# Performance work log

Measured on AMD Instinct MI355X. Metric: run time of the kernel, lower is better.

Reference implementation:

```python
import jax, jax.numpy as jnp
import numpy as np

B, T, C = 8, 1024, 1024
EPS = 1e-5
NEG_INF = -1e38


def layernorm(x, w, b):
    mu = jnp.mean(x, axis=-1, keepdims=True)
    var = jnp.var(x, axis=-1, keepdims=True)
    return (x - mu) * jax.lax.rsqrt(var + EPS) * w + b


def wkv_scan(w, u, k, v):
    """Numerically-stable RWKV-4 WKV recurrence (forward direction).
    w: [C] (negative decay), u: [C] bonus, k, v: [B, T, C]. Returns [B, T, C]."""
    kt = jnp.swapaxes(k, 0, 1)  # [T, B, C]
    vt = jnp.swapaxes(v, 0, 1)
    bsz = k.shape[0]
    a0 = jnp.zeros((bsz, C), k.dtype)
    b0 = jnp.zeros((bsz, C), k.dtype)
    p0 = jnp.full((bsz, C), NEG_INF, k.dtype)

    def step(carry, inp):
        a, b, p = carry
        kk, vv = inp
        # output at current step (with bonus u on current token)
        q = jnp.maximum(p, u + kk)
        e1 = jnp.exp(p - q)
        e2 = jnp.exp(u + kk - q)
        out = (e1 * a + e2 * vv) / (e1 * b + e2)
        # decay state and absorb current token
        q2 = jnp.maximum(p + w, kk)
        f1 = jnp.exp(p + w - q2)
        f2 = jnp.exp(kk - q2)
        return (f1 * a + f2 * vv, f1 * b + f2, q2), out

    _, outs = jax.lax.scan(step, (a0, b0, p0), (kt, vt))
    return jnp.swapaxes(outs, 0, 1)  # [B, T, C]


def setup_inputs() -> dict:
    key = jax.random.key(0)
    ks = jax.random.split(key, 12)
    s = 0.02
    d = {}
    d["x"] = jax.random.normal(ks[0], (B, T, C), jnp.float32)
    d["ln1_w"] = jnp.ones((C,), jnp.float32)
    d["ln1_b"] = jnp.zeros((C,), jnp.float32)
    d["ln2_w"] = jnp.ones((C,), jnp.float32)
    d["ln2_b"] = jnp.zeros((C,), jnp.float32)
    d["Wr"] = jax.random.normal(ks[1], (C, C), jnp.float32) * s
    d["Wk"] = jax.random.normal(ks[2], (C, C), jnp.float32) * s
    d["Wv"] = jax.random.normal(ks[3], (C, C), jnp.float32) * s
    d["Wo"] = jax.random.normal(ks[4], (C, C), jnp.float32) * s
    d["decay"] = jax.random.normal(ks[5], (C,), jnp.float32) * 0.1
    d["u"] = jax.random.normal(ks[6], (C,), jnp.float32) * 0.1
    d["Wfk"] = jax.random.normal(ks[7], (4 * C, C), jnp.float32) * s
    d["Wfv"] = jax.random.normal(ks[8], (C, 4 * C), jnp.float32) * s
    d["Wfr"] = jax.random.normal(ks[9], (C, C), jnp.float32) * s
    return d


def reference(x, ln1_w, ln1_b, ln2_w, ln2_b, Wr, Wk, Wv, Wo, decay, u, Wfk, Wfv, Wfr):
    # --- bidirectional time-mix (WKV attention) ---
    xn = layernorm(x, ln1_w, ln1_b)
    r = jax.nn.sigmoid(xn @ Wr.T)
    k = xn @ Wk.T
    v = xn @ Wv.T
    w = -jnp.exp(decay)  # per-channel negative decay
    wkv_f = wkv_scan(w, u, k, v)
    wkv_b = jnp.flip(wkv_scan(w, u, jnp.flip(k, axis=1), jnp.flip(v, axis=1)), axis=1)
    wkv = 0.5 * (wkv_f + wkv_b)
    x = x + (r * wkv) @ Wo.T
    # --- channel-mix FFN ---
    xn2 = layernorm(x, ln2_w, ln2_b)
    kk = jnp.square(jax.nn.relu(xn2 @ Wfk.T))  # [B, T, 4C]
    x = x + jax.nn.sigmoid(xn2 @ Wfr.T) * (kk @ Wfv.T)
    return x
```

## Files before the change

kernel.cpp:

```cpp
#include <hip/hip_runtime.h>
#include <cstdint>
#include <cstddef>

typedef unsigned short u16;
typedef unsigned char u8;
typedef unsigned int u32;
typedef __bf16 bf16_t;
typedef bf16_t bf16x8 __attribute__((ext_vector_type(8)));
typedef float f32x4 __attribute__((ext_vector_type(4)));
typedef int i32x8 __attribute__((ext_vector_type(8)));

#define GCH 16
#define TCH 64

static __device__ __forceinline__ float bf2f(u16 v) {
    union { unsigned int u; float f; } cv;
    cv.u = ((unsigned int)v) << 16;
    return cv.f;
}
static __device__ __forceinline__ u16 f2bf(float f) {
    union { float f; unsigned int u; } cv;
    cv.f = f;
    unsigned int r = 0x7fffu + ((cv.u >> 16) & 1u);
    return (u16)((cv.u + r) >> 16);
}

struct WSegs { const float* src[7]; void* dst[7]; int n4[7]; int mode[7]; };

__global__ __launch_bounds__(256)
void wconv_all(WSegs s)
{
    const int seg = blockIdx.y;
    const int i = blockIdx.x * 256 + threadIdx.x;
    if (i >= s.n4[seg]) return;
    float4 f = ((const float4*)s.src[seg])[i];
    if (s.mode[seg] == 0) {
        ushort4 o;
        o.x = f2bf(f.x); o.y = f2bf(f.y); o.z = f2bf(f.z); o.w = f2bf(f.w);
        ((ushort4*)s.dst[seg])[i] = o;
    } else {
        const int p0 = __builtin_amdgcn_cvt_pk_fp8_f32(f.x * 16.f, f.y * 16.f, 0, 0);
        const int p1 = __builtin_amdgcn_cvt_pk_fp8_f32(f.z * 16.f, f.w * 16.f, 0, 0);
        ((u32*)s.dst[seg])[i] = (u32)(p0 & 0xFFFF) | ((u32)p1 << 16);
    }
}

template<int BF16IN, int OUT8>
__global__ __launch_bounds__(256)
void ln_kernel(const void* __restrict__ xin, const float* __restrict__ w,
               const float* __restrict__ b, void* __restrict__ out)
{
    const int row = blockIdx.x;
    const int tid = threadIdx.x;
    float vals[4];
    if (BF16IN) {
        const ushort4 uv = ((const ushort4*)((const u16*)xin + (size_t)row * 1024))[tid];
        vals[0] = bf2f(uv.x); vals[1] = bf2f(uv.y);
        vals[2] = bf2f(uv.z); vals[3] = bf2f(uv.w);
    } else {
        const float4 f = ((const float4*)((const float*)xin + (size_t)row * 1024))[tid];
        vals[0] = f.x; vals[1] = f.y; vals[2] = f.z; vals[3] = f.w;
    }
    float s  = vals[0] + vals[1] + vals[2] + vals[3];
    float ss = vals[0]*vals[0] + vals[1]*vals[1] + vals[2]*vals[2] + vals[3]*vals[3];
    for (int off = 32; off; off >>= 1) {
        s  += __shfl_down(s, off, 64);
        ss += __shfl_down(ss, off, 64);
    }
    __shared__ float redS[4], redQ[4];
    if ((tid & 63) == 0) { redS[tid >> 6] = s; redQ[tid >> 6] = ss; }
    __syncthreads();
    s  = redS[0] + redS[1] + redS[2] + redS[3];
    ss = redQ[0] + redQ[1] + redQ[2] + redQ[3];
    const float mu  = s * (1.f / 1024.f);
    const float var = ss * (1.f / 1024.f) - mu * mu;
    const float rs  = rsqrtf(var + 1e-5f);
    const float4 wv = ((const float4*)w)[tid];
    const float4 bv = ((const float4*)b)[tid];
    const float o0 = (vals[0] - mu) * rs * wv.x + bv.x;
    const float o1 = (vals[1] - mu) * rs * wv.y + bv.y;
    const float o2 = (vals[2] - mu) * rs * wv.z + bv.z;
    const float o3 = (vals[3] - mu) * rs * wv.w + bv.w;
    if (OUT8) {
        const int p0 = __builtin_amdgcn_cvt_pk_fp8_f32(o0, o1, 0, 0);
        const int p1 = __builtin_amdgcn_cvt_pk_fp8_f32(o2, o3, 0, 0);
        ((u32*)out)[(size_t)row * 256 + tid] = (u32)(p0 & 0xFFFF) | ((u32)p1 << 16);
    } else {
        ushort4 o;
        o.x = f2bf(o0); o.y = f2bf(o1); o.z = f2bf(o2); o.w = f2bf(o3);
        ((ushort4*)out)[(size_t)row * 256 + tid] = o;
    }
}

template<int EPI, int DBUF>
__global__ __launch_bounds__(256)
void gemm_bt(const u16* __restrict__ A, const u16* __restrict__ B,
             int M, int N, int K,
             void* __restrict__ outp,
             const void* __restrict__ aux1, const void* __restrict__ aux2)
{
    __shared__ u16 lA[(1 + DBUF) * 128 * 64];
    __shared__ u16 lB[(1 + DBUF) * 128 * 64];
    const int tid  = threadIdx.x;
    const int wave = tid >> 6;
    const int lane = tid & 63;
    const int q    = lane >> 4;
    const int l16  = lane & 15;
    const long mBase = (long)blockIdx.x * 128;
    const long nBase = (long)blockIdx.y * 128;
    const int wm = (wave >> 1) * 64;
    const int wn = (wave & 1) * 64;

    f32x4 acc[4][4];
#pragma unroll
    for (int i = 0; i < 4; ++i)
#pragma unroll
        for (int j = 0; j < 4; ++j)
#pragma unroll
            for (int r = 0; r < 4; ++r) acc[i][j][r] = 0.f;

    const int srow = tid >> 3;
    const int scol = ((tid & 7) ^ (srow & 7)) * 8;
    const int ldsW = wave * 512;
    const int swz = l16 & 7;

    if (DBUF == 0) {
        for (int kb = 0; kb < K; kb += 64) {
            __syncthreads();
#pragma unroll
            for (int c = 0; c < 4; ++c) {
                const int row = c * 32 + srow;
                const u16* ga = A + (mBase + row) * (long)K + kb + scol;
                const u16* gb = B + (nBase + row) * (long)K + kb + scol;
                __builtin_amdgcn_global_load_lds(
                    (const __attribute__((address_space(1))) void*)ga,
                    (__attribute__((address_space(3))) void*)(lA + c * 2048 + ldsW),
                    16, 0, 0);
                __builtin_amdgcn_global_load_lds(
                    (const __attribute__((address_space(1))) void*)gb,
                    (__attribute__((address_space(3))) void*)(lB + c * 2048 + ldsW),
                    16, 0, 0);
            }
            __syncthreads();
#pragma unroll
            for (int ks = 0; ks < 2; ++ks) {
                const int grp = ((ks * 4 + q) ^ swz) * 8;
                bf16x8 af[4], bfm[4];
#pragma unroll
                for (int i = 0; i < 4; ++i) {
                    af[i]  = *(const bf16x8*)(lA + (wm + i * 16 + l16) * 64 + grp);
                    bfm[i] = *(const bf16x8*)(lB + (wn + i * 16 + l16) * 64 + grp);
                }
#pragma unroll
                for (int i = 0; i < 4; ++i)
#pragma unroll
                    for (int j = 0; j < 4; ++j)
                        acc[i][j] = __builtin_amdgcn_mfma_f32_16x16x32_bf16(
                            af[i], bfm[j], acc[i][j], 0, 0, 0);
            }
        }
    } else {
#pragma unroll
        for (int c = 0; c < 4; ++c) {
            const int row = c * 32 + srow;
            const u16* ga = A + (mBase + row) * (long)K + scol;
            const u16* gb = B + (nBase + row) * (long)K + scol;
            __builtin_amdgcn_global_load_lds(
                (const __attribute__((address_space(1))) void*)ga,
                (__attribute__((address_space(3))) void*)(lA + c * 2048 + ldsW),
                16, 0, 0);
            __builtin_amdgcn_global_load_lds(
                (const __attribute__((address_space(1))) void*)gb,
                (__attribute__((address_space(3))) void*)(lB + c * 2048 + ldsW),
                16, 0, 0);
        }
        __syncthreads();
        int cur = 0;
        for (int kb = 0; kb < K; kb += 64) {
            if (kb + 64 < K) {
                const int nb = (cur ^ 1) * 8192;
#pragma unroll
                for (int c = 0; c < 4; ++c) {
                    const int row = c * 32 + srow;
                    const u16* ga = A + (mBase + row) * (long)K + kb + 64 + scol;
                    const u16* gb = B + (nBase + row) * (long)K + kb + 64 + scol;
                    __builtin_amdgcn_global_load_lds(
                        (const __attribute__((address_space(1))) void*)ga,
                        (__attribute__((address_space(3))) void*)(lA + nb + c * 2048 + ldsW),
                        16, 0, 0);
                    __builtin_amdgcn_global_load_lds(
                        (const __attribute__((address_space(1))) void*)gb,
                        (__attribute__((address_space(3))) void*)(lB + nb + c * 2048 + ldsW),
                        16, 0, 0);
                }
            }
            const u16* bA = lA + cur * 8192;
            const u16* bB = lB + cur * 8192;
#pragma unroll
            for (int ks = 0; ks < 2; ++ks) {
                const int grp = ((ks * 4 + q) ^ swz) * 8;
                bf16x8 af[4], bfm[4];
#pragma unroll
                for (int i = 0; i < 4; ++i) {
                    af[i]  = *(const bf16x8*)(bA + (wm + i * 16 + l16) * 64 + grp);
                    bfm[i] = *(const bf16x8*)(bB + (wn + i * 16 + l16) * 64 + grp);
                }
#pragma unroll
                for (int i = 0; i < 4; ++i)
#pragma unroll
                    for (int j = 0; j < 4; ++j)
                        acc[i][j] = __builtin_amdgcn_mfma_f32_16x16x32_bf16(
                            af[i], bfm[j], acc[i][j], 0, 0, 0);
            }
            __syncthreads();
            cur ^= 1;
        }
    }

    if (EPI == 5) {
        const long seg = nBase >> 10;
        u16* optr = (u16*)(seg == 0 ? outp : seg == 1 ? (void*)aux1 : (void*)aux2);
        const long cb = (nBase & 1023) + wn + l16;
#pragma unroll
        for (int i = 0; i < 4; ++i)
#pragma unroll
            for (int r = 0; r < 4; ++r) {
                const long rowOff = (mBase + wm + i * 16 + q * 4 + r) * 1024 + cb;
#pragma unroll
                for (int j = 0; j < 4; ++j)
                    optr[rowOff + j * 16] = f2bf(acc[i][j][r]);
            }
    } else {
        const long colBase = nBase + wn + l16;
#pragma unroll
        for (int i = 0; i < 4; ++i) {
#pragma unroll
            for (int r = 0; r < 4; ++r) {
                const long row = mBase + wm + i * 16 + q * 4 + r;
                const long rowOff = row * (long)N;
#pragma unroll
                for (int j = 0; j < 4; ++j) {
                    const long idx = rowOff + colBase + j * 16;
                    const float val = acc[i][j][r];
                    if (EPI == 1) {
                        ((u16*)outp)[idx] = f2bf(((const float*)aux1)[idx] + val);
                    } else {
                        const float t = bf2f(((const u16*)aux1)[idx])
                                      + bf2f(((const u16*)aux2)[idx]) * val;
                        ((float*)outp)[idx] = t;
                    }
                }
            }
        }
    }
}

__global__ __launch_bounds__(256)
void gemm_f8(const u8* __restrict__ A, const u8* __restrict__ B,
             int M, int N, int K,
             u16* __restrict__ kk, u16* __restrict__ rp)
{
    __shared__ __align__(16) u8 lA[128 * 128];
    __shared__ __align__(16) u8 lB[128 * 128];
    const int tid  = threadIdx.x;
    const int wave = tid >> 6;
    const int lane = tid & 63;
    const int q    = lane >> 4;
    const int l16  = lane & 15;
    const long mBase = (long)blockIdx.x * 128;
    const long nBase = (long)blockIdx.y * 128;
    const int wm = (wave >> 1) * 64;
    const int wn = (wave & 1) * 64;

    f32x4 acc[4][4];
#pragma unroll
    for (int i = 0; i < 4; ++i)
#pragma unroll
        for (int j = 0; j < 4; ++j)
#pragma unroll
            for (int r = 0; r < 4; ++r) acc[i][j][r] = 0.f;

    const int srow  = tid >> 3;
    const int scolB = ((tid & 7) ^ (srow & 7)) * 16;
    const int ldsW  = wave * 1024;
    const int swz   = l16 & 7;

    for (int kb = 0; kb < K; kb += 128) {
        __syncthreads();
#pragma unroll
        for (int c = 0; c < 4; ++c) {
            const int row = c * 32 + srow;
            const u8* ga = A + (mBase + row) * (long)K + kb + scolB;
            const u8* gb = B + (nBase + row) * (long)K + kb + scolB;
            __builtin_amdgcn_global_load_lds(
                (const __attribute__((address_space(1))) void*)ga,
                (__attribute__((address_space(3))) void*)(lA + c * 4096 + ldsW),
                16, 0, 0);
            __builtin_amdgcn_global_load_lds(
                (const __attribute__((address_space(1))) void*)gb,
                (__attribute__((address_space(3))) void*)(lB + c * 4096 + ldsW),
                16, 0, 0);
        }
        __syncthreads();
        const int u0 = ((2 * q) ^ swz) * 16;
        const int u1 = ((2 * q + 1) ^ swz) * 16;
        i32x8 af[4], bfm[4];
#pragma unroll
        for (int i = 0; i < 4; ++i) {
            {
                const u8* base = lA + (wm + i * 16 + l16) * 128;
                const uint4 lo = *(const uint4*)(base + u0);
                const uint4 hi = *(const uint4*)(base + u1);
                af[i][0] = lo.x; af[i][1] = lo.y; af[i][2] = lo.z; af[i][3] = lo.w;
                af[i][4] = hi.x; af[i][5] = hi.y; af[i][6] = hi.z; af[i][7] = hi.w;
            }
            {
                const u8* base = lB + (wn + i * 16 + l16) * 128;
                const uint4 lo = *(const uint4*)(base + u0);
                const uint4 hi = *(const uint4*)(base + u1);
                bfm[i][0] = lo.x; bfm[i][1] = lo.y; bfm[i][2] = lo.z; bfm[i][3] = lo.w;
                bfm[i][4] = hi.x; bfm[i][5] = hi.y; bfm[i][6] = hi.z; bfm[i][7] = hi.w;
            }
        }
#pragma unroll
        for (int i = 0; i < 4; ++i)
#pragma unroll
            for (int j = 0; j < 4; ++j)
                acc[i][j] = __builtin_amdgcn_mfma_scale_f32_16x16x128_f8f6f4(
                    af[i], bfm[j], acc[i][j], 0, 0, 0, 127, 0, 123);
    }

    u16* optr; long sN, cb;
    if (nBase < 4096) { optr = kk; sN = 4096; cb = nBase + wn + l16; }
    else              { optr = rp; sN = 1024; cb = (nBase - 4096) + wn + l16; }
#pragma unroll
    for (int i = 0; i < 4; ++i)
#pragma unroll
        for (int r = 0; r < 4; ++r) {
            const long rowOff = (mBase + wm + i * 16 + q * 4 + r) * sN + cb;
#pragma unroll
            for (int j = 0; j < 4; ++j) {
                const float val = acc[i][j][r];
                float t;
                if (nBase < 4096) t = val > 0.f ? val * val : 0.f;
                else t = __fdividef(1.f, 1.f + __expf(-val));
                optr[rowOff + j * 16] = f2bf(t);
            }
        }
}

__global__ __launch_bounds__(64)
void wkv_sum(const u16* __restrict__ kbuf, const u16* __restrict__ vbuf,
             const float* __restrict__ decay,
             float* __restrict__ sumA, float* __restrict__ sumB,
             float* __restrict__ sumP)
{
    const int c   = blockIdx.x * 64 + threadIdx.x;
    const int bt  = blockIdx.y;
    const int dir = blockIdx.z & 1;
    const int g   = blockIdx.z >> 1;
    const long base = (long)bt * (1024 * 1024) + c;
    const long stride = dir ? -1024 : 1024;
    long idx = dir ? base + (long)(1023 - g * TCH) * 1024
                   : base + (long)(g * TCH) * 1024;
    const float w = -__expf(decay[c]);
    float a = 0.f, b = 0.f, p = -1e38f;

    float kq[8], vq[8];
#pragma unroll
    for (int j = 0; j < 8; ++j) {
        kq[j] = bf2f(kbuf[idx + j * stride]);
        vq[j] = bf2f(vbuf[idx + j * stride]);
    }
    for (int tb = 0; tb < TCH / 8; ++tb) {
        float kn[8], vn[8];
        if (tb < TCH / 8 - 1) {
#pragma unroll
            for (int j = 0; j < 8; ++j) {
                kn[j] = bf2f(kbuf[idx + (j + 8) * stride]);
                vn[j] = bf2f(vbuf[idx + (j + 8) * stride]);
            }
        }
#pragma unroll
        for (int j = 0; j < 8; ++j) {
            const float kk = kq[j], vv = vq[j];
            const float pw = p + w;
            const float d  = pw - kk;
            const float e  = __expf(-fabsf(d));
            const float f1 = d >= 0.f ? 1.f : e;
            const float f2 = d >= 0.f ? e : 1.f;
            a = f1 * a + f2 * vv;
            b = f1 * b + f2;
            p = fmaxf(pw, kk);
        }
#pragma unroll
        for (int j = 0; j < 8; ++j) { kq[j] = kn[j]; vq[j] = vn[j]; }
        idx += 8 * stride;
    }
    const int sidx = (((dir * GCH + g) * 8 + bt) << 10) + c;
    sumA[sidx] = a; sumB[sidx] = b; sumP[sidx] = p;
}

__global__ __launch_bounds__(64)
void wkv_out2(const u16* __restrict__ kbuf, const u16* __restrict__ vbuf,
              const float* __restrict__ decay, const float* __restrict__ uarr,
              const float* __restrict__ sumA, const float* __restrict__ sumB,
              const float* __restrict__ sumP,
              const u16* __restrict__ rpre, u16* __restrict__ rwkv)
{
    __shared__ float fbuf[TCH * 64];
    const int lane = threadIdx.x;
    const int c   = blockIdx.x * 64 + lane;
    const int bt  = blockIdx.y;
    const int g   = blockIdx.z;
    const long base = (long)bt * (1024 * 1024) + c;
    const long rowBase = base + (long)(g * TCH) * 1024;
    const float w  = -__expf(decay[c]);
    const float uu = uarr[c];

    {
        float a = 0.f, b = 0.f, p = -1e38f;
        for (int gg = 0; gg < g; ++gg) {
            const int sidx = ((gg * 8 + bt) << 10) + c;
            const float a2 = sumA[sidx], b2 = sumB[sidx], p2 = sumP[sidx];
            const float pd = p + w * (float)TCH;
            const float d  = pd - p2;
            const float e  = __expf(-fabsf(d));
            const float x1 = d >= 0.f ? 1.f : e;
            const float x2 = d >= 0.f ? e : 1.f;
            a = x1 * a + x2 * a2;
            b = x1 * b + x2 * b2;
            p = fmaxf(pd, p2);
        }
        long idx = rowBase;
        float kq[8], vq[8];
#pragma unroll
        for (int j = 0; j < 8; ++j) {
            kq[j] = bf2f(kbuf[idx + j * 1024]);
            vq[j] = bf2f(vbuf[idx + j * 1024]);
        }
        for (int tb = 0; tb < TCH / 8; ++tb) {
            float kn[8], vn[8];
            if (tb < TCH / 8 - 1) {
#pragma unroll
                for (int j = 0; j < 8; ++j) {
                    kn[j] = bf2f(kbuf[idx + (j + 8) * 1024]);
                    vn[j] = bf2f(vbuf[idx + (j + 8) * 1024]);
                }
            }
#pragma unroll
            for (int j = 0; j < 8; ++j) {
                const float kk = kq[j], vv = vq[j];
                const float uk = uu + kk;
                const float d1 = p - uk;
                const float e  = __expf(-fabsf(d1));
                const float e1 = d1 >= 0.f ? 1.f : e;
                const float e2 = d1 >= 0.f ? e : 1.f;
                fbuf[(tb * 8 + j) * 64 + lane] =
                    __fdividef(e1 * a + e2 * vv, e1 * b + e2);
                const float pw = p + w;
                const float d2 = pw - kk;
                const float e_ = __expf(-fabsf(d2));
                const float f1 = d2 >= 0.f ? 1.f : e_;
                const float f2 = d2 >= 0.f ? e_ : 1.f;
                a = f1 * a + f2 * vv;
                b = f1 * b + f2;
                p = fmaxf(pw, kk);
            }
#pragma unroll
            for (int j = 0; j < 8; ++j) { kq[j] = kn[j]; vq[j] = vn[j]; }
            idx += 8 * 1024;
        }
    }
    __syncthreads();

    {
        float a = 0.f, b = 0.f, p = -1e38f;
        const int gb = GCH - 1 - g;
        for (int gg = 0; gg < gb; ++gg) {
            const int sidx = (((GCH + gg) * 8 + bt) << 10) + c;
            const float a2 = sumA[sidx], b2 = sumB[sidx], p2 = sumP[sidx];
            const float pd = p + w * (float)TCH;
            const float d  = pd - p2;
            const float e  = __expf(-fabsf(d));
            const float x1 = d >= 0.f ? 1.f : e;
            const float x2 = d >= 0.f ? e : 1.f;
            a = x1 * a + x2 * a2;
            b = x1 * b + x2 * b2;
            p = fmaxf(pd, p2);
        }
        long idx = rowBase + (long)(TCH - 1) * 1024;
        float kq[8], vq[8];
#pragma unroll
        for (int j = 0; j < 8; ++j) {
            kq[j] = bf2f(kbuf[idx - j * 1024]);
            vq[j] = bf2f(vbuf[idx - j * 1024]);
        }
        for (int tb = 0; tb < TCH / 8; ++tb) {
            float kn[8], vn[8];
            if (tb < TCH / 8 - 1) {
#pragma unroll
                for (int j = 0; j < 8; ++j) {
                    kn[j] = bf2f(kbuf[idx - (j + 8) * 1024]);
                    vn[j] = bf2f(vbuf[idx - (j + 8) * 1024]);
                }
            }
#pragma unroll
            for (int j = 0; j < 8; ++j) {
                const long ii = idx - (long)j * 1024;
                const int  tl = TCH - 1 - (tb * 8 + j);
                const float kk = kq[j], vv = vq[j];
                const float uk = uu + kk;
                const float d1 = p - uk;
                const float e  = __expf(-fabsf(d1));
                const float e1 = d1 >= 0.f ? 1.f : e;
                const float e2 = d1 >= 0.f ? e : 1.f;
                const float ob = __fdividef(e1 * a + e2 * vv, e1 * b + e2);
                const float of = fbuf[tl * 64 + lane];
                const float rr = __fdividef(1.f, 1.f + __expf(-bf2f(rpre[ii])));
                rwkv[ii] = f2bf(rr * 0.5f * (of + ob));
                const float pw = p + w;
                const float d2 = pw - kk;
                const float e_ = __expf(-fabsf(d2));
                const float f1 = d2 >= 0.f ? 1.f : e_;
                const float f2 = d2 >= 0.f ? e_ : 1.f;
                a = f1 * a + f2 * vv;
                b = f1 * b + f2;
                p = fmaxf(pw, kk);
            }
#pragma unroll
            for (int j = 0; j < 8; ++j) { kq[j] = kn[j]; vq[j] = vn[j]; }
            idx -= 8 * 1024;
        }
    }
}

extern "C" void kernel_launch(void* const* d_in, const int* in_sizes, int n_in,
                              void* d_out, int out_size, void* d_ws, size_t ws_size,
                              hipStream_t stream)
{
    (void)in_sizes; (void)n_in; (void)out_size; (void)ws_size;
    const float* x     = (const float*)d_in[0];
    const float* ln1w  = (const float*)d_in[1];
    const float* ln1b  = (const float*)d_in[2];
    const float* ln2w  = (const float*)d_in[3];
    const float* ln2b  = (const float*)d_in[4];
    const float* Wr    = (const float*)d_in[5];
    const float* Wk    = (const float*)d_in[6];
    const float* Wv    = (const float*)d_in[7];
    const float* Wo    = (const float*)d_in[8];
    const float* decay = (const float*)d_in[9];
    const float* uarr  = (const float*)d_in[10];
    const float* Wfk   = (const float*)d_in[11];
    const float* Wfv   = (const float*)d_in[12];
    const float* Wfr   = (const float*)d_in[13];

    const int M = 8192, C = 1024, C4 = 4096;
    const size_t MB = 1024u * 1024u;
    char* ws = (char*)d_ws;
    u16*  X2    = (u16*)(ws);
    u16*  XN    = (u16*)(ws + 16 * MB);
    u8*   XN8   = (u8*)(ws + 16 * MB);
    u16*  RP    = (u16*)(ws + 32 * MB);
    u16*  KB    = (u16*)(ws + 48 * MB);
    u16*  VB    = (u16*)(ws + 64 * MB);
    u16*  RWKV  = (u16*)(ws + 80 * MB);
    u16*  KK    = (u16*)(ws + 48 * MB);
    float* sumA = (float*)(ws + 112 * MB);
    float* sumB = (float*)(ws + 113 * MB);
    float* sumP = (float*)(ws + 114 * MB);
    u16*  WrB   = (u16*)(ws + 116 * MB);
    u16*  WkB   = (u16*)(ws + 118 * MB);
    u16*  WvB   = (u16*)(ws + 120 * MB);
    u16*  WoB   = (u16*)(ws + 122 * MB);
    u8*   Wf8   = (u8*)(ws + 124 * MB);
    u8*   Wfr8  = (u8*)(ws + 128 * MB);
    u16*  WfvB  = (u16*)(ws + 130 * MB);

    const dim3 blk(256);
    const int n4_1M = C * C / 4, n4_4M = C * C4 / 4;

    WSegs segs;
    segs.src[0] = Wr;  segs.dst[0] = WrB;  segs.n4[0] = n4_1M; segs.mode[0] = 0;
    segs.src[1] = Wk;  segs.dst[1] = WkB;  segs.n4[1] = n4_1M; segs.mode[1] = 0;
    segs.src[2] = Wv;  segs.dst[2] = WvB;  segs.n4[2] = n4_1M; segs.mode[2] = 0;
    segs.src[3] = Wo;  segs.dst[3] = WoB;  segs.n4[3] = n4_1M; segs.mode[3] = 0;
    segs.src[4] = Wfk; segs.dst[4] = Wf8;  segs.n4[4] = n4_4M; segs.mode[4] = 1;
    segs.src[5] = Wfr; segs.dst[5] = Wfr8; segs.n4[5] = n4_1M; segs.mode[5] = 1;
    segs.src[6] = Wfv; segs.dst[6] = WfvB; segs.n4[6] = n4_4M; segs.mode[6] = 0;
    wconv_all<<<dim3(n4_4M / 256, 7), blk, 0, stream>>>(segs);

    ln_kernel<0, 0><<<dim3(M), blk, 0, stream>>>(x, ln1w, ln1b, XN);
    gemm_bt<5, 0><<<dim3(M / 128, 3 * C / 128), blk, 0, stream>>>(
        XN, WrB, M, 3 * C, C, RP, KB, VB);
    wkv_sum<<<dim3(16, 8, 2 * GCH), dim3(64), 0, stream>>>(KB, VB, decay,
                                                           sumA, sumB, sumP);
    wkv_out2<<<dim3(16, 8, GCH), dim3(64), 0, stream>>>(KB, VB, decay, uarr,
                                                        sumA, sumB, sumP,
                                                        RP, RWKV);
    gemm_bt<1, 1><<<dim3(M / 128, C / 128), blk, 0, stream>>>(
        RWKV, WoB, M, C, C, X2, x, nullptr);
    ln_kernel<1, 1><<<dim3(M), blk, 0, stream>>>(X2, ln2w, ln2b, XN8);
    gemm_f8<<<dim3(M / 128, 5 * C / 128), blk, 0, stream>>>(
        XN8, Wf8, M, 5 * C, C, KK, RP);
    gemm_bt<4, 1><<<dim3(M / 128, C / 128), blk, 0, stream>>>(
        KK, WfvB, M, C, C4, d_out, X2, RP);
}
```

Baseline: 406.3 us.

## Restructure bf16 GEMM double-buffer pipeline with partial vmcnt waits

The double-buffered bf16 GEMM main loop is rewritten as stage/compute lambdas. Two K-tiles are kept in flight at once, and the loop uses `s_waitcnt vmcnt(8)` plus raw `s_barrier` with sched barriers instead of `__syncthreads`. The aim is to stop draining every outstanding global-to-LDS load each iteration, so loads overlap better with MFMA work. The fused QKV projection GEMM is also switched to this pipelined variant through its template flag. The explicit waitcnt counts depend on each stage issuing exactly eight loads per thread, so the code is fragile if the tile shape changes.

```diff
diff --git a/kernel.cpp b/kernel.cpp
--- a/kernel.cpp
+++ b/kernel.cpp
@@ -24,6 +24,10 @@
     unsigned int r = 0x7fffu + ((cv.u >> 16) & 1u);
     return (u16)((cv.u + r) >> 16);
 }
+
+#define SBAR() do { __builtin_amdgcn_sched_barrier(0); \
+                    __builtin_amdgcn_s_barrier();      \
+                    __builtin_amdgcn_sched_barrier(0); } while (0)
 
 struct WSegs { const float* src[7]; void* dst[7]; int n4[7]; int mode[7]; };
 
@@ -160,42 +164,25 @@
             }
         }
     } else {
-#pragma unroll
-        for (int c = 0; c < 4; ++c) {
-            const int row = c * 32 + srow;
-            const u16* ga = A + (mBase + row) * (long)K + scol;
-            const u16* gb = B + (nBase + row) * (long)K + scol;
-            __builtin_amdgcn_global_load_lds(
-                (const __attribute__((address_space(1))) void*)ga,
-                (__attribute__((address_space(3))) void*)(lA + c * 2048 + ldsW),
-                16, 0, 0);
-            __builtin_amdgcn_global_load_lds(
-                (const __attribute__((address_space(1))) void*)gb,
-                (__attribute__((address_space(3))) void*)(lB + c * 2048 + ldsW),
-                16, 0, 0);
-        }
-        __syncthreads();
-        int cur = 0;
-        for (int kb = 0; kb < K; kb += 64) {
-            if (kb + 64 < K) {
-                const int nb = (cur ^ 1) * 8192;
-#pragma unroll
-                for (int c = 0; c < 4; ++c) {
-                    const int row = c * 32 + srow;
-                    const u16* ga = A + (mBase + row) * (long)K + kb + 64 + scol;
-                    const u16* gb = B + (nBase + row) * (long)K + kb + 64 + scol;
-                    __builtin_amdgcn_global_load_lds(
-                        (const __attribute__((address_space(1))) void*)ga,
-                        (__attribute__((address_space(3))) void*)(lA + nb + c * 2048 + ldsW),
-                        16, 0, 0);
-                    __builtin_amdgcn_global_load_lds(
-                        (const __attribute__((address_space(1))) void*)gb,
-                        (__attribute__((address_space(3))) void*)(lB + nb + c * 2048 + ldsW),
-                        16, 0, 0);
-                }
-            }
-            const u16* bA = lA + cur * 8192;
-            const u16* bB = lB + cur * 8192;
+        auto stage = [&](int kb, int bufsel) {
+#pragma unroll
+            for (int c = 0; c < 4; ++c) {
+                const int row = c * 32 + srow;
+                const u16* ga = A + (mBase + row) * (long)K + kb + scol;
+                const u16* gb = B + (nBase + row) * (long)K + kb + scol;
+                __builtin_amdgcn_global_load_lds(
+                    (const __attribute__((address_space(1))) void*)ga,
+                    (__attribute__((address_space(3))) void*)(lA + bufsel * 8192 + c * 2048 + ldsW),
+                    16, 0, 0);
+                __builtin_amdgcn_global_load_lds(
+                    (const __attribute__((address_space(1))) void*)gb,
+                    (__attribute__((address_space(3))) void*)(lB + bufsel * 8192 + c * 2048 + ldsW),
+                    16, 0, 0);
+            }
+        };
+        auto compute = [&](int bufsel) {
+            const u16* bA = lA + bufsel * 8192;
+            const u16* bB = lB + bufsel * 8192;
 #pragma unroll
             for (int ks = 0; ks < 2; ++ks) {
                 const int grp = ((ks * 4 + q) ^ swz) * 8;
@@ -212,9 +199,24 @@
                         acc[i][j] = __builtin_amdgcn_mfma_f32_16x16x32_bf16(
                             af[i], bfm[j], acc[i][j], 0, 0, 0);
             }
-            __syncthreads();
-            cur ^= 1;
-        }
+        };
+
+        const int nt = K >> 6;
+        stage(0, 0);
+        stage(64, 1);
+        asm volatile("s_waitcnt vmcnt(8)" ::: "memory");
+        SBAR();
+        for (int t = 0; t < nt - 2; ++t) {
+            compute(t & 1);
+            SBAR();
+            stage((t + 2) << 6, t & 1);
+            asm volatile("s_waitcnt vmcnt(8)" ::: "memory");
+            SBAR();
+        }
+        compute(nt & 1);
+        asm volatile("s_waitcnt vmcnt(0)" ::: "memory");
+        SBAR();
+        compute((nt - 1) & 1);
     }
 
     if (EPI == 5) {
@@ -591,7 +593,7 @@
     wconv_all<<<dim3(n4_4M / 256, 7), blk, 0, stream>>>(segs);
 
     ln_kernel<0, 0><<<dim3(M), blk, 0, stream>>>(x, ln1w, ln1b, XN);
-    gemm_bt<5, 0><<<dim3(M / 128, 3 * C / 128), blk, 0, stream>>>(
+    gemm_bt<5, 1><<<dim3(M / 128, 3 * C / 128), blk, 0, stream>>>(
         XN, WrB, M, 3 * C, C, RP, KB, VB);
     wkv_sum<<<dim3(16, 8, 2 * GCH), dim3(64), 0, stream>>>(KB, VB, decay,
                                                            sumA, sumB, sumP);
```

Measured after the change: 418.5 us. 3.0% more time.
